# Kernel tuning notes

Measured on AMD Instinct MI355X. Metric: run time of the kernel, lower is better.

## Reference

```python
import jax, jax.numpy as jnp
import numpy as np

NEG_SLOPE = 0.2


def setup_inputs() -> dict:
    key = jax.random.key(0)
    k1, k2, k3 = jax.random.split(key, 3)
    bs, n_agents, input_dim = 32, 512, 128
    n_heads, hidden_dim = 8, 64
    h = jax.random.normal(k1, (bs, n_agents, input_dim), dtype=jnp.float32)
    # Linear(input_dim, n_heads*hidden_dim, bias=False), stored as [in, out]
    W = jax.random.normal(k2, (input_dim, n_heads * hidden_dim), dtype=jnp.float32) * (1.0 / np.sqrt(input_dim))
    # xavier_uniform with gain=1.414 on shape (1, n_heads, 2*hidden_dim)
    fan = n_heads + 2 * hidden_dim
    bound = 1.414 * np.sqrt(6.0 / fan)
    att_a = jax.random.uniform(k3, (1, n_heads, 2 * hidden_dim), dtype=jnp.float32,
                               minval=-bound, maxval=bound)
    return {"h": h, "W": W, "att_a": att_a}


def reference(h, W, att_a):
    bs, n_agents, _ = h.shape
    n_heads = att_a.shape[1]
    hidden_dim = att_a.shape[2] // 2
    # h_prime: [bs, n_heads, n_agents, hidden_dim]
    h_prime = (h @ W).reshape(bs, n_agents, n_heads, hidden_dim).transpose(0, 2, 1, 3)
    # Additive score decomposes exactly: (a1.h_i + a2.h_j) == sum(cat(h_i,h_j)*a)
    a_src = att_a[0, :, :hidden_dim]   # [n_heads, hidden_dim]
    a_dst = att_a[0, :, hidden_dim:]   # [n_heads, hidden_dim]
    e_src = jnp.einsum('bhnd,hd->bhn', h_prime, a_src)  # score contribution of node i (row)
    e_dst = jnp.einsum('bhnd,hd->bhn', h_prime, a_dst)  # contribution of node j (col)
    e = e_src[:, :, :, None] + e_dst[:, :, None, :]     # [bs, n_heads, n, n]
    e = jnp.where(e >= 0, e, NEG_SLOPE * e)             # leaky_relu(0.2)
    attention = jax.nn.softmax(e, axis=-1)
    h_new = jnp.einsum('bhnm,bhmd->bhnd', attention, h_prime)
    return jax.nn.elu(h_new)
```

## Files before the change

### kernel.cpp

```cpp
#include <hip/hip_runtime.h>

#define BS 32
#define NA 512
#define ID 128
#define NH 8
#define HD 64
#define NHD 512
#define NEG 0.2f
#define NC 32
#define CH 16
#define TROWS (NA + 1)

__global__ __launch_bounds__(256) void k1_gemm(
    const float* __restrict__ h, const float* __restrict__ W,
    const float* __restrict__ att, float* __restrict__ hp,
    float* __restrict__ s_out, float* __restrict__ t_out) {
  int blk = blockIdx.x;
  int b = blk >> 5;
  int n0 = (blk & 31) * 16;
  int t = threadIdx.x;
  int lane = t & 63, w = t >> 6;
  int r0 = __builtin_amdgcn_readfirstlane((w >> 1) * 8);
  int chalf = __builtin_amdgcn_readfirstlane(w & 1);
  int col = chalf * 256 + lane * 4;
  int head = col >> 6;
  int d0 = col & 63;
  const float* arow = h + ((size_t)b * NA + n0 + r0) * ID;
  const float* wptr = W + col;

  float4 a0c = {0,0,0,0}, a1c = {0,0,0,0}, a2c = {0,0,0,0}, a3c = {0,0,0,0};
  float4 a4c = {0,0,0,0}, a5c = {0,0,0,0}, a6c = {0,0,0,0}, a7c = {0,0,0,0};

#define K1_ROW(I, C, KK)                                                      \
  { float a_ = arow[(I) * ID + kc + (KK)];                                    \
    C.x += a_ * wv.x; C.y += a_ * wv.y; C.z += a_ * wv.z; C.w += a_ * wv.w; }
  #pragma unroll 1
  for (int kc = 0; kc < ID; kc += 8) {
    #pragma unroll
    for (int kk = 0; kk < 8; ++kk) {
      float4 wv = *(const float4*)(wptr + (size_t)(kc + kk) * NHD);
      K1_ROW(0, a0c, kk) K1_ROW(1, a1c, kk) K1_ROW(2, a2c, kk)
      K1_ROW(3, a3c, kk) K1_ROW(4, a4c, kk) K1_ROW(5, a5c, kk)
      K1_ROW(6, a6c, kk) K1_ROW(7, a7c, kk)
    }
  }
#undef K1_ROW
  {
    size_t off = ((((size_t)b * NH + head) * NA) + (n0 + r0)) * HD + d0;
    *(float4*)(hp + off) = a0c; off += HD;
    *(float4*)(hp + off) = a1c; off += HD;
    *(float4*)(hp + off) = a2c; off += HD;
    *(float4*)(hp + off) = a3c; off += HD;
    *(float4*)(hp + off) = a4c; off += HD;
    *(float4*)(hp + off) = a5c; off += HD;
    *(float4*)(hp + off) = a6c; off += HD;
    *(float4*)(hp + off) = a7c;
  }
  {
    float4 as4 = *(const float4*)(att + head * 128 + d0);
    float4 ad4 = *(const float4*)(att + head * 128 + 64 + d0);
#define DOT4(C, A) ((C).x*(A).x + (C).y*(A).y + (C).z*(A).z + (C).w*(A).w)
    float sp0 = DOT4(a0c, as4), tp0 = DOT4(a0c, ad4);
    float sp1 = DOT4(a1c, as4), tp1 = DOT4(a1c, ad4);
    float sp2 = DOT4(a2c, as4), tp2 = DOT4(a2c, ad4);
    float sp3 = DOT4(a3c, as4), tp3 = DOT4(a3c, ad4);
    float sp4 = DOT4(a4c, as4), tp4 = DOT4(a4c, ad4);
    float sp5 = DOT4(a5c, as4), tp5 = DOT4(a5c, ad4);
    float sp6 = DOT4(a6c, as4), tp6 = DOT4(a6c, ad4);
    float sp7 = DOT4(a7c, as4), tp7 = DOT4(a7c, ad4);
#undef DOT4
    #pragma unroll
    for (int m = 1; m < 16; m <<= 1) {
      sp0 += __shfl_xor(sp0, m, 64); tp0 += __shfl_xor(tp0, m, 64);
      sp1 += __shfl_xor(sp1, m, 64); tp1 += __shfl_xor(tp1, m, 64);
      sp2 += __shfl_xor(sp2, m, 64); tp2 += __shfl_xor(tp2, m, 64);
      sp3 += __shfl_xor(sp3, m, 64); tp3 += __shfl_xor(tp3, m, 64);
      sp4 += __shfl_xor(sp4, m, 64); tp4 += __shfl_xor(tp4, m, 64);
      sp5 += __shfl_xor(sp5, m, 64); tp5 += __shfl_xor(tp5, m, 64);
      sp6 += __shfl_xor(sp6, m, 64); tp6 += __shfl_xor(tp6, m, 64);
      sp7 += __shfl_xor(sp7, m, 64); tp7 += __shfl_xor(tp7, m, 64);
    }
    int g16 = lane & 15;
    int rsel = g16 & 7;
    float sv_ = rsel == 0 ? sp0 : rsel == 1 ? sp1 : rsel == 2 ? sp2 :
                rsel == 3 ? sp3 : rsel == 4 ? sp4 : rsel == 5 ? sp5 :
                rsel == 6 ? sp6 : sp7;
    float tv_ = rsel == 0 ? tp0 : rsel == 1 ? tp1 : rsel == 2 ? tp2 :
                rsel == 3 ? tp3 : rsel == 4 ? tp4 : rsel == 5 ? tp5 :
                rsel == 6 ? tp6 : tp7;
    size_t off = (((size_t)b * NH + head) * NA) + n0 + r0 + rsel;
    if (g16 < 8) s_out[off] = sv_;
    else         t_out[off] = tv_;
  }
}

__global__ __launch_bounds__(512) void k2a_tables(
    const float* __restrict__ hp, const float* __restrict__ s_g,
    const float* __restrict__ t_g, float* __restrict__ sufPfull,
    float* __restrict__ preNfull, float4* __restrict__ rinfo_g) {
  __shared__ float tv[NA]; __shared__ int tpm[NA];
  __shared__ float wp[NA]; __shared__ float wn[NA];
  __shared__ float rawP[NC * 64]; __shared__ float rawN[NC * 64];
  __shared__ float sufP[(NC + 1) * 64]; __shared__ float preN[(NC + 1) * 64];
  __shared__ float zps[NA + 1]; __shared__ float znp[NA + 1];
  __shared__ float szP[NC]; __shared__ float szN[NC];
  __shared__ float sufZ[NC + 1]; __shared__ float preZ[NC + 1];
  __shared__ float smax8[8];

  int bh = blockIdx.x;
  int t = threadIdx.x;
  int lane = t & 63, w = t >> 6;
  const float* vbase = hp + (size_t)bh * NA * HD;

  float v = t_g[(size_t)bh * NA + t];
  int idx = t;
  for (int size = 2; size <= NA; size <<= 1) {
    bool dirAsc = ((t & size) == 0);
    for (int stride = size >> 1; stride > 0; stride >>= 1) {
      float pv; int pi;
      if (stride >= 64) {
        tv[t] = v; tpm[t] = idx;
        __syncthreads();
        pv = tv[t ^ stride]; pi = tpm[t ^ stride];
        __syncthreads();
      } else {
        pv = __shfl_xor(v, stride, 64);
        pi = __shfl_xor(idx, stride, 64);
      }
      bool mn = (((t & stride) == 0) == dirAsc);
      bool sw = mn ? (pv < v) : (pv > v);
      if (sw) { v = pv; idx = pi; }
    }
  }
  tv[t] = v; tpm[t] = idx;
  __syncthreads();

  float cmax = fmaxf(tv[NA - 1], 0.f);
  wp[t] = __expf(tv[t] - cmax);
  wn[t] = __expf(NEG * tv[t] - cmax);
  float sval = s_g[(size_t)bh * NA + t];
  {
    float m = sval;
    #pragma unroll
    for (int d = 32; d; d >>= 1) m = fmaxf(m, __shfl_xor(m, d, 64));
    if (lane == 0) smax8[w] = m;
  }
  __syncthreads();
  float amax = fmaxf(fmaxf(fmaxf(smax8[0], smax8[1]), fmaxf(smax8[2], smax8[3])),
                     fmaxf(fmaxf(smax8[4], smax8[5]), fmaxf(smax8[6], smax8[7])));
  amax = fmaxf(amax, 0.f);

  {
    for (int cc = w; cc < NC; cc += 8) {
      float aP = 0.f, aN = 0.f;
      #pragma unroll
      for (int jj = 0; jj < CH; ++jj) {
        int j = cc * CH + jj;
        float vv = vbase[(size_t)tpm[j] * HD + lane];
        aP += wp[j] * vv;
        aN += wn[j] * vv;
      }
      rawP[cc * 64 + lane] = aP;
      rawN[cc * 64 + lane] = aN;
    }
  }
  __syncthreads();

  if (t < 64) {
    int d = t; float run = 0.f;
    sufP[NC * 64 + d] = 0.f;
    for (int cc = NC - 1; cc >= 0; --cc) { run += rawP[cc * 64 + d]; sufP[cc * 64 + d] = run; }
  } else if (t < 128) {
    int d = t - 64; float run = 0.f;
    for (int cc = 0; cc <= NC; ++cc) { preN[cc * 64 + d] = run; if (cc < NC) run += rawN[cc * 64 + d]; }
  } else if (t < 160) {
    int c = t - 128; float a = 0.f;
    for (int j = c * CH; j < c * CH + CH; ++j) a += wp[j];
    szP[c] = a;
  } else if (t < 192) {
    int c = t - 160; float a = 0.f;
    for (int j = c * CH; j < c * CH + CH; ++j) a += wn[j];
    szN[c] = a;
  }
  __syncthreads();

  if (t == 0) {
    float run = 0.f; sufZ[NC] = 0.f;
    for (int cc = NC - 1; cc >= 0; --cc) { run += szP[cc]; sufZ[cc] = run; }
  } else if (t == 1) {
    float run = 0.f;
    for (int cc = 0; cc <= NC; ++cc) { preZ[cc] = run; if (cc < NC) run += szN[cc]; }
  }
  __syncthreads();

  {
    int ch = t >> 4;
    float a = 0.f;
    for (int k = t; k < ch * CH + CH; ++k) a += wp[k];
    zps[t] = a + sufZ[ch + 1];
    float b2 = 0.f;
    for (int k = ch * CH; k < t; ++k) b2 += wn[k];
    znp[t] = preZ[ch] + b2;
    if (t == 0) { zps[NA] = 0.f; znp[NA] = preZ[NC]; }
  }
  __syncthreads();

  {
    float* sP = sufPfull + (size_t)bh * TROWS * 64;
    float* pN = preNfull + (size_t)bh * TROWS * 64;
    int jbase = w * 64;
    float run = sufP[(w * 4 + 4) * 64 + lane];
    for (int jj = 63; jj >= 0; --jj) {
      int j = jbase + jj;
      float vv = vbase[(size_t)tpm[j] * HD + lane];
      run += wp[j] * vv;
      sP[(size_t)j * 64 + lane] = run;
    }
    float run2 = preN[(w * 4) * 64 + lane];
    for (int jj = 0; jj < 64; ++jj) {
      int j = jbase + jj;
      pN[(size_t)j * 64 + lane] = run2;
      float vv = vbase[(size_t)tpm[j] * HD + lane];
      run2 += wn[j] * vv;
    }
    if (t < 64) {
      sP[(size_t)NA * 64 + t] = 0.f;
      pN[(size_t)NA * 64 + t] = preN[NC * 64 + t];
    }
  }

  {
    float A = __expf(sval - amax);
    float B = __expf(NEG * sval - amax);
    float key = -sval;
    int lo = 0, hi = NA;
    while (lo < hi) { int mid = (lo + hi) >> 1; if (tv[mid] < key) lo = mid + 1; else hi = mid; }
    int js = lo;
    float den = A * zps[js] + B * znp[js];
    float4 ri;
    ri.x = A; ri.y = B; ri.z = 1.f / den; ri.w = __int_as_float(js);
    rinfo_g[(size_t)bh * NA + t] = ri;
  }
}

__global__ __launch_bounds__(256) void k2b_apply(
    const float* __restrict__ sufPfull, const float* __restrict__ preNfull,
    const float4* __restrict__ rinfo_g, float* __restrict__ out) {
  int blk = blockIdx.x;
  int bh = blk >> 7;
  int row = (blk & 127) * 4 + (threadIdx.x >> 6);
  int lane = threadIdx.x & 63;
  float4 ri = rinfo_g[(size_t)bh * NA + row];
  int js = __float_as_int(ri.w);
  size_t tb = ((size_t)bh * TROWS + js) * 64 + lane;
  float x = (ri.x * sufPfull[tb] + ri.y * preNfull[tb]) * ri.z;
  out[(((size_t)bh * NA) + row) * 64 + lane] = x > 0.f ? x : __expf(x) - 1.f;
}

__global__ __launch_bounds__(512) void k2_fallback(
    const float* __restrict__ hp, const float* __restrict__ s_g,
    const float* __restrict__ t_g, float* __restrict__ out) {
  __shared__ float tv[NA]; __shared__ int tpm[NA];
  __shared__ float sv[NA]; __shared__ int spm[NA];
  __shared__ float wp[NA]; __shared__ float wn[NA];
  __shared__ float rawP[NC * 64]; __shared__ float rawN[NC * 64];
  __shared__ float sufP[(NC + 1) * 64]; __shared__ float preN[(NC + 1) * 64];
  __shared__ float zps[NA + 1]; __shared__ float znp[NA + 1];
  __shared__ float szP[NC]; __shared__ float szN[NC];
  __shared__ float sufZ[NC + 1]; __shared__ float preZ[NC + 1];
  int bh = blockIdx.x;
  int t = threadIdx.x;
  const float* vbase = hp + (size_t)bh * NA * HD;
  tv[t] = t_g[(size_t)bh * NA + t]; tpm[t] = t;
  sv[t] = s_g[(size_t)bh * NA + t]; spm[t] = t;
  __syncthreads();
  for (int size = 2; size <= NA; size <<= 1) {
    for (int stride = size >> 1; stride > 0; stride >>= 1) {
      int i = t, j = i ^ stride;
      if (j > i) {
        bool up = ((i & size) == 0);
        float a = tv[i], b = tv[j];
        if (up ? (a > b) : (a < b)) {
          tv[i] = b; tv[j] = a;
          int x = tpm[i]; tpm[i] = tpm[j]; tpm[j] = x;
        }
        float c = sv[i], d = sv[j];
        if (up ? (c > d) : (c < d)) {
          sv[i] = d; sv[j] = c;
          int x = spm[i]; spm[i] = spm[j]; spm[j] = x;
        }
      }
      __syncthreads();
    }
  }
  float cmax = fmaxf(tv[NA - 1], 0.f);
  float amax = fmaxf(sv[NA - 1], 0.f);
  wp[t] = __expf(tv[t] - cmax);
  wn[t] = __expf(NEG * tv[t] - cmax);
  __syncthreads();
  {
    int d = t & 63, w8 = t >> 6;
    for (int cc = w8; cc < NC; cc += 8) {
      float aP = 0.f, aN = 0.f;
      #pragma unroll
      for (int jj = 0; jj < CH; ++jj) {
        int j = cc * CH + jj;
        float vv = vbase[(size_t)tpm[j] * HD + d];
        aP += wp[j] * vv;
        aN += wn[j] * vv;
      }
      rawP[cc * 64 + d] = aP;
      rawN[cc * 64 + d] = aN;
    }
  }
  __syncthreads();
  if (t < 64) {
    int d = t; float run = 0.f;
    sufP[NC * 64 + d] = 0.f;
    for (int cc = NC - 1; cc >= 0; --cc) { run += rawP[cc * 64 + d]; sufP[cc * 64 + d] = run; }
  } else if (t < 128) {
    int d = t - 64; float run = 0.f;
    for (int cc = 0; cc <= NC; ++cc) { preN[cc * 64 + d] = run; if (cc < NC) run += rawN[cc * 64 + d]; }
  } else if (t < 160) {
    int c = t - 128; float a = 0.f;
    for (int j = c * CH; j < c * CH + CH; ++j) a += wp[j];
    szP[c] = a;
  } else if (t < 192) {
    int c = t - 160; float a = 0.f;
    for (int j = c * CH; j < c * CH + CH; ++j) a += wn[j];
    szN[c] = a;
  }
  __syncthreads();
  if (t == 0) {
    float run = 0.f; sufZ[NC] = 0.f;
    for (int cc = NC - 1; cc >= 0; --cc) { run += szP[cc]; sufZ[cc] = run; }
  } else if (t == 1) {
    float run = 0.f;
    for (int cc = 0; cc <= NC; ++cc) { preZ[cc] = run; if (cc < NC) run += szN[cc]; }
  }
  __syncthreads();
  {
    int ch = t >> 4;
    float a = 0.f;
    for (int k = t; k < ch * CH + CH; ++k) a += wp[k];
    zps[t] = a + sufZ[ch + 1];
    float b2 = 0.f;
    for (int k = ch * CH; k < t; ++k) b2 += wn[k];
    znp[t] = preZ[ch] + b2;
    if (t == 0) { zps[NA] = 0.f; znp[NA] = preZ[NC]; }
  }
  __syncthreads();
  {
    float sval = sv[t];
    int row = spm[t];
    float A = __expf(sval - amax);
    float B = __expf(NEG * sval - amax);
    float key = -sval;
    int lo = 0, hi = NA;
    while (lo < hi) { int mid = (lo + hi) >> 1; if (tv[mid] < key) lo = mid + 1; else hi = mid; }
    int js = lo;
    int cs = js >> 4; if (cs > NC - 1) cs = NC - 1;
    float den = A * zps[js] + B * znp[js];
    float inv = 1.f / den;
    const float* sp_ = &sufP[(cs + 1) * 64];
    const float* pn_ = &preN[cs * 64];
    float* ob = out + ((size_t)bh * NA + row) * HD;
#define INIT4(P) { float4 aa = *(const float4*)(sp_ + (P));                   \
                   float4 bb = *(const float4*)(pn_ + (P));                   \
                   nn.x = A*aa.x + B*bb.x; nn.y = A*aa.y + B*bb.y;            \
                   nn.z = A*aa.z + B*bb.z; nn.w = A*aa.w + B*bb.w; }
#define LD_FMA(NN, P) { float4 vv = *(const float4*)(vrow + (P));             \
                        NN.x += coef*vv.x; NN.y += coef*vv.y;                 \
                        NN.z += coef*vv.z; NN.w += coef*vv.w; }
#define ELU_ST(NN, P) { float4 ov;                                            \
                        float x0 = NN.x*inv; ov.x = x0>0.f?x0:__expf(x0)-1.f; \
                        float x1 = NN.y*inv; ov.y = x1>0.f?x1:__expf(x1)-1.f; \
                        float x2 = NN.z*inv; ov.z = x2>0.f?x2:__expf(x2)-1.f; \
                        float x3 = NN.w*inv; ov.w = x3>0.f?x3:__expf(x3)-1.f; \
                        *(float4*)(ob + (P)) = ov; }
    #pragma unroll
    for (int half = 0; half < 2; ++half) {
      int ho = half * 32;
      float4 n0, n1, n2, n3, n4, n5, n6, n7;
      { float4 nn; INIT4(ho +  0) n0 = nn; INIT4(ho +  4) n1 = nn;
                   INIT4(ho +  8) n2 = nn; INIT4(ho + 12) n3 = nn;
                   INIT4(ho + 16) n4 = nn; INIT4(ho + 20) n5 = nn;
                   INIT4(ho + 24) n6 = nn; INIT4(ho + 28) n7 = nn; }
      #pragma unroll 2
      for (int jj = 0; jj < CH; ++jj) {
        int j = cs * CH + jj;
        float coef = (j >= js) ? A * wp[j] : B * wn[j];
        const float* vrow = vbase + (size_t)tpm[j] * HD + ho;
        LD_FMA(n0,  0) LD_FMA(n1,  4) LD_FMA(n2,  8) LD_FMA(n3, 12)
        LD_FMA(n4, 16) LD_FMA(n5, 20) LD_FMA(n6, 24) LD_FMA(n7, 28)
      }
      ELU_ST(n0, ho +  0) ELU_ST(n1, ho +  4) ELU_ST(n2, ho +  8)
      ELU_ST(n3, ho + 12) ELU_ST(n4, ho + 16) ELU_ST(n5, ho + 20)
      ELU_ST(n6, ho + 24) ELU_ST(n7, ho + 28)
    }
#undef INIT4
#undef LD_FMA
#undef ELU_ST
  }
}

extern "C" void kernel_launch(void* const* d_in, const int* in_sizes, int n_in,
                              void* d_out, int out_size, void* d_ws, size_t ws_size,
                              hipStream_t stream) {
  const float* h  = (const float*)d_in[0];
  const float* W  = (const float*)d_in[1];
  const float* att = (const float*)d_in[2];
  float* out = (float*)d_out;
  float* hp    = (float*)d_ws;
  float* s_arr = hp + (size_t)BS * NH * NA * HD;
  float* t_arr = s_arr + (size_t)BS * NH * NA;
  float* sufPf = t_arr + (size_t)BS * NH * NA;
  float* preNf = sufPf + (size_t)BS * NH * TROWS * 64;
  float* rinfo = preNf + (size_t)BS * NH * TROWS * 64;
  size_t need_floats = (size_t)BS * NH * NA * HD + 2 * (size_t)BS * NH * NA +
                       2 * (size_t)BS * NH * TROWS * 64 + (size_t)BS * NH * NA * 4;
  size_t need = need_floats * sizeof(float);

  k1_gemm<<<dim3(1024), dim3(256), 0, stream>>>(h, W, att, hp, s_arr, t_arr);
  if (ws_size >= need) {
    k2a_tables<<<dim3(256),   dim3(512), 0, stream>>>(hp, s_arr, t_arr, sufPf,
                                                      preNf, (float4*)rinfo);
    k2b_apply <<<dim3(32768), dim3(256), 0, stream>>>(sufPf, preNf,
                                                      (float4*)rinfo, out);
  } else {
    k2_fallback<<<dim3(256), dim3(512), 0, stream>>>(hp, s_arr, t_arr, out);
  }
}
```

Baseline: 149.1 us.

## Fuse table build and apply into one kernel that scatters output rows during prefix sweep

```diff
diff --git a/kernel.cpp b/kernel.cpp
--- a/kernel.cpp
+++ b/kernel.cpp
@@ -9,7 +9,7 @@
 #define NEG 0.2f
 #define NC 32
 #define CH 16
-#define TROWS (NA + 1)
+#define NW 8
 
 __global__ __launch_bounds__(256) void k1_gemm(
     const float* __restrict__ h, const float* __restrict__ W,
@@ -94,85 +94,84 @@
   }
 }
 
-__global__ __launch_bounds__(512) void k2a_tables(
+__global__ __launch_bounds__(512, 2) void k2_fused(
     const float* __restrict__ hp, const float* __restrict__ s_g,
-    const float* __restrict__ t_g, float* __restrict__ sufPfull,
-    float* __restrict__ preNfull, float4* __restrict__ rinfo_g) {
+    const float* __restrict__ t_g, float* __restrict__ out) {
   __shared__ float tv[NA]; __shared__ int tpm[NA];
+  __shared__ float sv[NA]; __shared__ int spm[NA];
   __shared__ float wp[NA]; __shared__ float wn[NA];
-  __shared__ float rawP[NC * 64]; __shared__ float rawN[NC * 64];
-  __shared__ float sufP[(NC + 1) * 64]; __shared__ float preN[(NC + 1) * 64];
+  __shared__ float rawP8[NW * 64]; __shared__ float rawN8[NW * 64];
+  __shared__ float sufPc[(NW + 1) * 64]; __shared__ float preNc[(NW + 1) * 64];
   __shared__ float zps[NA + 1]; __shared__ float znp[NA + 1];
   __shared__ float szP[NC]; __shared__ float szN[NC];
   __shared__ float sufZ[NC + 1]; __shared__ float preZ[NC + 1];
-  __shared__ float smax8[8];
+  __shared__ float4 abi[NA];
+  __shared__ int jsr[NA];
+  __shared__ int Earr[NA];
 
   int bh = blockIdx.x;
   int t = threadIdx.x;
   int lane = t & 63, w = t >> 6;
   const float* vbase = hp + (size_t)bh * NA * HD;
 
-  float v = t_g[(size_t)bh * NA + t];
-  int idx = t;
+  float vt = t_g[(size_t)bh * NA + t]; int it = t;
+  float vs = s_g[(size_t)bh * NA + t]; int is_ = t;
   for (int size = 2; size <= NA; size <<= 1) {
     bool dirAsc = ((t & size) == 0);
     for (int stride = size >> 1; stride > 0; stride >>= 1) {
-      float pv; int pi;
+      float pt, ps; int pit, pis;
       if (stride >= 64) {
-        tv[t] = v; tpm[t] = idx;
+        tv[t] = vt; tpm[t] = it; sv[t] = vs; spm[t] = is_;
         __syncthreads();
-        pv = tv[t ^ stride]; pi = tpm[t ^ stride];
+        pt = tv[t ^ stride]; pit = tpm[t ^ stride];
+        ps = sv[t ^ stride]; pis = spm[t ^ stride];
         __syncthreads();
       } else {
-        pv = __shfl_xor(v, stride, 64);
-        pi = __shfl_xor(idx, stride, 64);
+        pt = __shfl_xor(vt, stride, 64); pit = __shfl_xor(it, stride, 64);
+        ps = __shfl_xor(vs, stride, 64); pis = __shfl_xor(is_, stride, 64);
       }
       bool mn = (((t & stride) == 0) == dirAsc);
-      bool sw = mn ? (pv < v) : (pv > v);
-      if (sw) { v = pv; idx = pi; }
-    }
-  }
-  tv[t] = v; tpm[t] = idx;
+      if (mn ? (pt < vt) : (pt > vt)) { vt = pt; it = pit; }
+      if (mn ? (ps < vs) : (ps > vs)) { vs = ps; is_ = pis; }
+    }
+  }
+  tv[t] = vt; tpm[t] = it; sv[t] = vs; spm[t] = is_;
   __syncthreads();
 
   float cmax = fmaxf(tv[NA - 1], 0.f);
-  wp[t] = __expf(tv[t] - cmax);
-  wn[t] = __expf(NEG * tv[t] - cmax);
-  float sval = s_g[(size_t)bh * NA + t];
-  {
-    float m = sval;
-    #pragma unroll
-    for (int d = 32; d; d >>= 1) m = fmaxf(m, __shfl_xor(m, d, 64));
-    if (lane == 0) smax8[w] = m;
-  }
-  __syncthreads();
-  float amax = fmaxf(fmaxf(fmaxf(smax8[0], smax8[1]), fmaxf(smax8[2], smax8[3])),
-                     fmaxf(fmaxf(smax8[4], smax8[5]), fmaxf(smax8[6], smax8[7])));
-  amax = fmaxf(amax, 0.f);
-
-  {
-    for (int cc = w; cc < NC; cc += 8) {
-      float aP = 0.f, aN = 0.f;
-      #pragma unroll
-      for (int jj = 0; jj < CH; ++jj) {
-        int j = cc * CH + jj;
-        float vv = vbase[(size_t)tpm[j] * HD + lane];
-        aP += wp[j] * vv;
-        aN += wn[j] * vv;
-      }
-      rawP[cc * 64 + lane] = aP;
-      rawN[cc * 64 + lane] = aN;
-    }
+  float amax = fmaxf(sv[NA - 1], 0.f);
+  wp[t] = __expf(vt - cmax);
+  wn[t] = __expf(NEG * vt - cmax);
+  __syncthreads();
+
+  float vreg[64];
+  {
+    float aP = 0.f, aN = 0.f;
+    #pragma unroll
+    for (int jj = 0; jj < 64; ++jj) {
+      int j = (w << 6) + jj;
+      float vv = vbase[(size_t)tpm[j] * HD + lane];
+      vreg[jj] = vv;
+      aP += wp[j] * vv;
+      aN += wn[j] * vv;
+    }
+    rawP8[(w << 6) + lane] = aP;
+    rawN8[(w << 6) + lane] = aN;
   }
   __syncthreads();
 
   if (t < 64) {
     int d = t; float run = 0.f;
-    sufP[NC * 64 + d] = 0.f;
-    for (int cc = NC - 1; cc >= 0; --cc) { run += rawP[cc * 64 + d]; sufP[cc * 64 + d] = run; }
+    sufPc[NW * 64 + d] = 0.f;
+    for (int ww = NW - 1; ww >= 0; --ww) {
+      run += rawP8[ww * 64 + d]; sufPc[ww * 64 + d] = run;
+    }
   } else if (t < 128) {
     int d = t - 64; float run = 0.f;
-    for (int cc = 0; cc <= NC; ++cc) { preN[cc * 64 + d] = run; if (cc < NC) run += rawN[cc * 64 + d]; }
+    for (int ww = 0; ww <= NW; ++ww) {
+      preNc[ww * 64 + d] = run;
+      if (ww < NW) run += rawN8[ww * 64 + d];
+    }
   } else if (t < 160) {
     int c = t - 128; float a = 0.f;
     for (int j = c * CH; j < c * CH + CH; ++j) a += wp[j];
@@ -206,228 +205,70 @@
   __syncthreads();
 
   {
-    float* sP = sufPfull + (size_t)bh * TROWS * 64;
-    float* pN = preNfull + (size_t)bh * TROWS * 64;
-    int jbase = w * 64;
-    float run = sufP[(w * 4 + 4) * 64 + lane];
-    for (int jj = 63; jj >= 0; --jj) {
-      int j = jbase + jj;
-      float vv = vbase[(size_t)tpm[j] * HD + lane];
-      run += wp[j] * vv;
-      sP[(size_t)j * 64 + lane] = run;
-    }
-    float run2 = preN[(w * 4) * 64 + lane];
-    for (int jj = 0; jj < 64; ++jj) {
-      int j = jbase + jj;
-      pN[(size_t)j * 64 + lane] = run2;
-      float vv = vbase[(size_t)tpm[j] * HD + lane];
-      run2 += wn[j] * vv;
-    }
-    if (t < 64) {
-      sP[(size_t)NA * 64 + t] = 0.f;
-      pN[(size_t)NA * 64 + t] = preN[NC * 64 + t];
-    }
-  }
-
-  {
-    float A = __expf(sval - amax);
-    float B = __expf(NEG * sval - amax);
-    float key = -sval;
+    float A = __expf(vs - amax);
+    float B = __expf(NEG * vs - amax);
+    float key = -vs;
     int lo = 0, hi = NA;
     while (lo < hi) { int mid = (lo + hi) >> 1; if (tv[mid] < key) lo = mid + 1; else hi = mid; }
-    int js = lo;
-    float den = A * zps[js] + B * znp[js];
-    float4 ri;
-    ri.x = A; ri.y = B; ri.z = 1.f / den; ri.w = __int_as_float(js);
-    rinfo_g[(size_t)bh * NA + t] = ri;
-  }
-}
-
-__global__ __launch_bounds__(256) void k2b_apply(
-    const float* __restrict__ sufPfull, const float* __restrict__ preNfull,
-    const float4* __restrict__ rinfo_g, float* __restrict__ out) {
-  int blk = blockIdx.x;
-  int bh = blk >> 7;
-  int row = (blk & 127) * 4 + (threadIdx.x >> 6);
-  int lane = threadIdx.x & 63;
-  float4 ri = rinfo_g[(size_t)bh * NA + row];
-  int js = __float_as_int(ri.w);
-  size_t tb = ((size_t)bh * TROWS + js) * 64 + lane;
-  float x = (ri.x * sufPfull[tb] + ri.y * preNfull[tb]) * ri.z;
-  out[(((size_t)bh * NA) + row) * 64 + lane] = x > 0.f ? x : __expf(x) - 1.f;
-}
-
-__global__ __launch_bounds__(512) void k2_fallback(
-    const float* __restrict__ hp, const float* __restrict__ s_g,
-    const float* __restrict__ t_g, float* __restrict__ out) {
-  __shared__ float tv[NA]; __shared__ int tpm[NA];
-  __shared__ float sv[NA]; __shared__ int spm[NA];
-  __shared__ float wp[NA]; __shared__ float wn[NA];
-  __shared__ float rawP[NC * 64]; __shared__ float rawN[NC * 64];
-  __shared__ float sufP[(NC + 1) * 64]; __shared__ float preN[(NC + 1) * 64];
-  __shared__ float zps[NA + 1]; __shared__ float znp[NA + 1];
-  __shared__ float szP[NC]; __shared__ float szN[NC];
-  __shared__ float sufZ[NC + 1]; __shared__ float preZ[NC + 1];
-  int bh = blockIdx.x;
-  int t = threadIdx.x;
-  const float* vbase = hp + (size_t)bh * NA * HD;
-  tv[t] = t_g[(size_t)bh * NA + t]; tpm[t] = t;
-  sv[t] = s_g[(size_t)bh * NA + t]; spm[t] = t;
-  __syncthreads();
-  for (int size = 2; size <= NA; size <<= 1) {
-    for (int stride = size >> 1; stride > 0; stride >>= 1) {
-      int i = t, j = i ^ stride;
-      if (j > i) {
-        bool up = ((i & size) == 0);
-        float a = tv[i], b = tv[j];
-        if (up ? (a > b) : (a < b)) {
-          tv[i] = b; tv[j] = a;
-          int x = tpm[i]; tpm[i] = tpm[j]; tpm[j] = x;
-        }
-        float c = sv[i], d = sv[j];
-        if (up ? (c > d) : (c < d)) {
-          sv[i] = d; sv[j] = c;
-          int x = spm[i]; spm[i] = spm[j]; spm[j] = x;
-        }
+    float den = A * zps[lo] + B * znp[lo];
+    float4 q; q.x = A; q.y = B; q.z = 1.f / den; q.w = __int_as_float(is_);
+    abi[t] = q;
+    jsr[t] = lo;
+  }
+  __syncthreads();
+
+  {
+    int lo = 0, hi = NA;
+    while (lo < hi) { int mid = (lo + hi) >> 1; if (jsr[mid] > t) lo = mid + 1; else hi = mid; }
+    Earr[t] = lo;
+  }
+  __syncthreads();
+
+  {
+    float sufPv = sufPc[w * 64 + lane];
+    float preSeedN = preNc[w * 64 + lane];
+    float runN = 0.f;
+    size_t obase = (size_t)bh * NA * HD + lane;
+    int eprev = (w == 0) ? NA : Earr[(w << 6) - 1];
+    #pragma unroll
+    for (int jj = 0; jj < 64; ++jj) {
+      int j = (w << 6) + jj;
+      int ecur = Earr[j];
+      float preNv = preSeedN + runN;
+      for (int r = ecur; r < eprev; ++r) {
+        float4 q = abi[r];
+        float x = (q.x * sufPv + q.y * preNv) * q.z;
+        int orow = __float_as_int(q.w);
+        out[obase + (size_t)orow * HD] = x > 0.f ? x : __expf(x) - 1.f;
       }
-      __syncthreads();
-    }
-  }
-  float cmax = fmaxf(tv[NA - 1], 0.f);
-  float amax = fmaxf(sv[NA - 1], 0.f);
-  wp[t] = __expf(tv[t] - cmax);
-  wn[t] = __expf(NEG * tv[t] - cmax);
-  __syncthreads();
-  {
-    int d = t & 63, w8 = t >> 6;
-    for (int cc = w8; cc < NC; cc += 8) {
-      float aP = 0.f, aN = 0.f;
-      #pragma unroll
-      for (int jj = 0; jj < CH; ++jj) {
-        int j = cc * CH + jj;
-        float vv = vbase[(size_t)tpm[j] * HD + d];
-        aP += wp[j] * vv;
-        aN += wn[j] * vv;
+      float vv = vreg[jj];
+      sufPv -= wp[j] * vv;
+      runN  += wn[j] * vv;
+      eprev = ecur;
+    }
+    if (w == NW - 1) {
+      float preNv = preSeedN + runN;
+      for (int r = 0; r < eprev; ++r) {
+        float4 q = abi[r];
+        float x = (q.y * preNv) * q.z;
+        int orow = __float_as_int(q.w);
+        out[obase + (size_t)orow * HD] = x > 0.f ? x : __expf(x) - 1.f;
       }
-      rawP[cc * 64 + d] = aP;
-      rawN[cc * 64 + d] = aN;
-    }
-  }
-  __syncthreads();
-  if (t < 64) {
-    int d = t; float run = 0.f;
-    sufP[NC * 64 + d] = 0.f;
-    for (int cc = NC - 1; cc >= 0; --cc) { run += rawP[cc * 64 + d]; sufP[cc * 64 + d] = run; }
-  } else if (t < 128) {
-    int d = t - 64; float run = 0.f;
-    for (int cc = 0; cc <= NC; ++cc) { preN[cc * 64 + d] = run; if (cc < NC) run += rawN[cc * 64 + d]; }
-  } else if (t < 160) {
-    int c = t - 128; float a = 0.f;
-    for (int j = c * CH; j < c * CH + CH; ++j) a += wp[j];
-    szP[c] = a;
-  } else if (t < 192) {
-    int c = t - 160; float a = 0.f;
-    for (int j = c * CH; j < c * CH + CH; ++j) a += wn[j];
-    szN[c] = a;
-  }
-  __syncthreads();
-  if (t == 0) {
-    float run = 0.f; sufZ[NC] = 0.f;
-    for (int cc = NC - 1; cc >= 0; --cc) { run += szP[cc]; sufZ[cc] = run; }
-  } else if (t == 1) {
-    float run = 0.f;
-    for (int cc = 0; cc <= NC; ++cc) { preZ[cc] = run; if (cc < NC) run += szN[cc]; }
-  }
-  __syncthreads();
-  {
-    int ch = t >> 4;
-    float a = 0.f;
-    for (int k = t; k < ch * CH + CH; ++k) a += wp[k];
-    zps[t] = a + sufZ[ch + 1];
-    float b2 = 0.f;
-    for (int k = ch * CH; k < t; ++k) b2 += wn[k];
-    znp[t] = preZ[ch] + b2;
-    if (t == 0) { zps[NA] = 0.f; znp[NA] = preZ[NC]; }
-  }
-  __syncthreads();
-  {
-    float sval = sv[t];
-    int row = spm[t];
-    float A = __expf(sval - amax);
-    float B = __expf(NEG * sval - amax);
-    float key = -sval;
-    int lo = 0, hi = NA;
-    while (lo < hi) { int mid = (lo + hi) >> 1; if (tv[mid] < key) lo = mid + 1; else hi = mid; }
-    int js = lo;
-    int cs = js >> 4; if (cs > NC - 1) cs = NC - 1;
-    float den = A * zps[js] + B * znp[js];
-    float inv = 1.f / den;
-    const float* sp_ = &sufP[(cs + 1) * 64];
-    const float* pn_ = &preN[cs * 64];
-    float* ob = out + ((size_t)bh * NA + row) * HD;
-#define INIT4(P) { float4 aa = *(const float4*)(sp_ + (P));                   \
-                   float4 bb = *(const float4*)(pn_ + (P));                   \
-                   nn.x = A*aa.x + B*bb.x; nn.y = A*aa.y + B*bb.y;            \
-                   nn.z = A*aa.z + B*bb.z; nn.w = A*aa.w + B*bb.w; }
-#define LD_FMA(NN, P) { float4 vv = *(const float4*)(vrow + (P));             \
-                        NN.x += coef*vv.x; NN.y += coef*vv.y;                 \
-                        NN.z += coef*vv.z; NN.w += coef*vv.w; }
-#define ELU_ST(NN, P) { float4 ov;                                            \
-                        float x0 = NN.x*inv; ov.x = x0>0.f?x0:__expf(x0)-1.f; \
-                        float x1 = NN.y*inv; ov.y = x1>0.f?x1:__expf(x1)-1.f; \
-                        float x2 = NN.z*inv; ov.z = x2>0.f?x2:__expf(x2)-1.f; \
-                        float x3 = NN.w*inv; ov.w = x3>0.f?x3:__expf(x3)-1.f; \
-                        *(float4*)(ob + (P)) = ov; }
-    #pragma unroll
-    for (int half = 0; half < 2; ++half) {
-      int ho = half * 32;
-      float4 n0, n1, n2, n3, n4, n5, n6, n7;
-      { float4 nn; INIT4(ho +  0) n0 = nn; INIT4(ho +  4) n1 = nn;
-                   INIT4(ho +  8) n2 = nn; INIT4(ho + 12) n3 = nn;
-                   INIT4(ho + 16) n4 = nn; INIT4(ho + 20) n5 = nn;
-                   INIT4(ho + 24) n6 = nn; INIT4(ho + 28) n7 = nn; }
-      #pragma unroll 2
-      for (int jj = 0; jj < CH; ++jj) {
-        int j = cs * CH + jj;
-        float coef = (j >= js) ? A * wp[j] : B * wn[j];
-        const float* vrow = vbase + (size_t)tpm[j] * HD + ho;
-        LD_FMA(n0,  0) LD_FMA(n1,  4) LD_FMA(n2,  8) LD_FMA(n3, 12)
-        LD_FMA(n4, 16) LD_FMA(n5, 20) LD_FMA(n6, 24) LD_FMA(n7, 28)
-      }
-      ELU_ST(n0, ho +  0) ELU_ST(n1, ho +  4) ELU_ST(n2, ho +  8)
-      ELU_ST(n3, ho + 12) ELU_ST(n4, ho + 16) ELU_ST(n5, ho + 20)
-      ELU_ST(n6, ho + 24) ELU_ST(n7, ho + 28)
-    }
-#undef INIT4
-#undef LD_FMA
-#undef ELU_ST
+    }
   }
 }
 
 extern "C" void kernel_launch(void* const* d_in, const int* in_sizes, int n_in,
                               void* d_out, int out_size, void* d_ws, size_t ws_size,
                               hipStream_t stream) {
-  const float* h  = (const float*)d_in[0];
-  const float* W  = (const float*)d_in[1];
+  const float* h   = (const float*)d_in[0];
+  const float* W   = (const float*)d_in[1];
   const float* att = (const float*)d_in[2];
   float* out = (float*)d_out;
   float* hp    = (float*)d_ws;
   float* s_arr = hp + (size_t)BS * NH * NA * HD;
   float* t_arr = s_arr + (size_t)BS * NH * NA;
-  float* sufPf = t_arr + (size_t)BS * NH * NA;
-  float* preNf = sufPf + (size_t)BS * NH * TROWS * 64;
-  float* rinfo = preNf + (size_t)BS * NH * TROWS * 64;
-  size_t need_floats = (size_t)BS * NH * NA * HD + 2 * (size_t)BS * NH * NA +
-                       2 * (size_t)BS * NH * TROWS * 64 + (size_t)BS * NH * NA * 4;
-  size_t need = need_floats * sizeof(float);
-
-  k1_gemm<<<dim3(1024), dim3(256), 0, stream>>>(h, W, att, hp, s_arr, t_arr);
-  if (ws_size >= need) {
-    k2a_tables<<<dim3(256),   dim3(512), 0, stream>>>(hp, s_arr, t_arr, sufPf,
-                                                      preNf, (float4*)rinfo);
-    k2b_apply <<<dim3(32768), dim3(256), 0, stream>>>(sufPf, preNf,
-                                                      (float4*)rinfo, out);
-  } else {
-    k2_fallback<<<dim3(256), dim3(512), 0, stream>>>(hp, s_arr, t_arr, out);
-  }
+
+  k1_gemm <<<dim3(1024), dim3(256), 0, stream>>>(h, W, att, hp, s_arr, t_arr);
+  k2_fused<<<dim3(BS * NH), dim3(512), 0, stream>>>(hp, s_arr, t_arr, out);
 }
```

Result: faster. 133.3 us (-10.6%).
